# Performance work log

Hardware: AMD Instinct MI355X
Metric: run time of the kernel (lower is better)

Reference implementation:

```python
import jax, jax.numpy as jnp
import numpy as np

# Static config (init_kwargs)
H = 56; W = 56; C = 256; NH = 8; WS = 7; SS = 3
HD = C // NH
SCALE = HD ** -0.5
N = WS * WS                      # tokens per window = 49
NW = (H // WS) * (W // WS)       # windows per image = 64
HIDDEN = int(C * 4.0)
EPS = 1e-5


def _rel_pos_index():
    coords = np.stack(np.meshgrid(np.arange(WS), np.arange(WS), indexing='ij')).reshape(2, -1)
    rel = coords[:, :, None] - coords[:, None, :]          # [2, N, N]
    rel = rel.transpose(1, 2, 0).astype(np.int64)          # [N, N, 2]
    rel[:, :, 0] += WS - 1
    rel[:, :, 1] += WS - 1
    rel[:, :, 0] *= 2 * WS - 1
    return rel.sum(-1).reshape(-1)                         # [N*N]


def _attn_mask():
    # (0 / -100) mask for the shifted-window configuration, [NW, N, N]
    img = np.zeros([H, W])
    cnt = 0
    for hs in (slice(0, -WS), slice(-WS, -SS), slice(-SS, None)):
        for ws in (slice(0, -WS), slice(-WS, -SS), slice(-SS, None)):
            img[hs, ws] = cnt
            cnt += 1
    mw = img.reshape(H // WS, WS, W // WS, WS).transpose(0, 2, 1, 3).reshape(-1, N)
    diff = mw[:, None, :] - mw[:, :, None]                 # [NW, N, N]
    return np.where(diff != 0, -100.0, 0.0).astype(np.float32)


_REL_IDX = _rel_pos_index()
_MASK = _attn_mask()


def _ln(x, g, b):
    mu = jnp.mean(x, axis=-1, keepdims=True)
    var = jnp.mean((x - mu) ** 2, axis=-1, keepdims=True)
    return (x - mu) * jax.lax.rsqrt(var + EPS) * g + b


def setup_inputs() -> dict:
    key = jax.random.key(0)
    ks = jax.random.split(key, 16)
    B = 32
    s = 0.02
    return {
        'x': jax.random.normal(ks[0], (B, H * W, C), dtype=jnp.float32),
        'gamma1': jnp.ones((C,), jnp.float32),
        'beta1': jnp.zeros((C,), jnp.float32),
        'qkv_w': jax.random.normal(ks[1], (C, 3 * C), jnp.float32) * s,
        'qkv_b': jnp.zeros((3 * C,), jnp.float32),
        'proj_w': jax.random.normal(ks[2], (C, C), jnp.float32) * s,
        'proj_b': jnp.zeros((C,), jnp.float32),
        'rpb_table': jax.random.normal(ks[3], ((2 * WS - 1) * (2 * WS - 1), NH), jnp.float32) * s,
        'gamma2': jnp.ones((C,), jnp.float32),
        'beta2': jnp.zeros((C,), jnp.float32),
        'fc1_w': jax.random.normal(ks[4], (C, HIDDEN), jnp.float32) * s,
        'fc1_b': jnp.zeros((HIDDEN,), jnp.float32),
        'fc2_w': jax.random.normal(ks[5], (HIDDEN, C), jnp.float32) * s,
        'fc2_b': jnp.zeros((C,), jnp.float32),
    }


def reference(x, gamma1, beta1, qkv_w, qkv_b, proj_w, proj_b, rpb_table,
              gamma2, beta2, fc1_w, fc1_b, fc2_w, fc2_b):
    B = x.shape[0]
    y = _ln(x, gamma1, beta1).reshape(B, H, W, C)
    # cyclic shift
    y = jnp.roll(y, (-SS, -SS), axis=(1, 2))
    # window partition -> [B*NW, N, C]
    win = y.reshape(B, H // WS, WS, W // WS, WS, C)
    win = win.transpose(0, 1, 3, 2, 4, 5).reshape(-1, N, C)
    # qkv projection, split heads
    qkv = (win @ qkv_w + qkv_b).reshape(-1, N, 3, NH, HD).transpose(2, 0, 3, 1, 4)
    q, k, v = qkv[0] * SCALE, qkv[1], qkv[2]            # [B*NW, NH, N, HD]
    attn = jnp.einsum('bhnd,bhmd->bhnm', q, k)          # [B*NW, NH, N, N]
    # gathered relative position bias
    bias = rpb_table[jnp.asarray(_REL_IDX)].reshape(N, N, NH).transpose(2, 0, 1)
    attn = attn + bias[None]
    # shift mask
    mask = jnp.asarray(_MASK)                           # [NW, N, N]
    attn = attn.reshape(B, NW, NH, N, N) + mask[None, :, None]
    attn = jax.nn.softmax(attn.reshape(-1, NH, N, N), axis=-1)
    o = jnp.einsum('bhnm,bhmd->bnhd', attn, v).reshape(-1, N, C)
    o = o @ proj_w + proj_b
    # window reverse + reverse shift
    o = o.reshape(B, H // WS, W // WS, WS, WS, C).transpose(0, 1, 3, 2, 4, 5).reshape(B, H, W, C)
    o = jnp.roll(o, (SS, SS), axis=(1, 2)).reshape(B, H * W, C)
    x = x + o
    # MLP block
    y = _ln(x, gamma2, beta2)
    y = jax.nn.gelu(y @ fc1_w + fc1_b, approximate=False) @ fc2_w + fc2_b
    return x + y
```

## Files before the change

### kernel.cpp

```cpp
#include <hip/hip_runtime.h>
#include <hip/hip_bf16.h>
#include <math.h>


typedef __bf16 bf16_t;
typedef __bf16 bf16x4 __attribute__((ext_vector_type(4)));
typedef __bf16 bf16x8 __attribute__((ext_vector_type(8)));
typedef float f32x4 __attribute__((ext_vector_type(4)));

#define AS1 __attribute__((address_space(1)))
#define AS3 __attribute__((address_space(3)))

__device__ __forceinline__ void gload_lds16(const bf16_t* g, bf16_t* l) {
  __builtin_amdgcn_global_load_lds((AS1 void*)g, (AS3 void*)l, 16, 0, 0);
}

__global__ void transpose_cast3(const float* __restrict__ qkv_w,
                                const float* __restrict__ proj_w,
                                const float* __restrict__ fc1_w,
                                bf16_t* __restrict__ qkvWt,
                                bf16_t* __restrict__ projWt,
                                bf16_t* __restrict__ fc1Wt) {
  int idx = blockIdx.x * 256 + threadIdx.x;
  const float* w;
  bf16_t* wt;
  int N;
  if (blockIdx.y == 0) { w = qkv_w; wt = qkvWt; N = 768; }
  else if (blockIdx.y == 1) { w = proj_w; wt = projWt; N = 256; }
  else { w = fc1_w; wt = fc1Wt; N = 1024; }
  if (idx < N * 256) {
    int n = idx >> 8, k = idx & 255;
    wt[idx] = (bf16_t)w[(size_t)k * N + n];
  }
}

__global__ void transpose_cast(const float* __restrict__ w, bf16_t* __restrict__ wt,
                               int K, int N) {
  int idx = blockIdx.x * 256 + threadIdx.x;
  if (idx < N * K) {
    int n = idx / K, k = idx - n * K;
    wt[idx] = (bf16_t)w[(size_t)k * N + n];
  }
}

__global__ void build_bm(const float* __restrict__ rpb, float* __restrict__ bm) {
  int t = blockIdx.x, h = blockIdx.y;
  int wr = (t & 2) ? 7 : 0, wc = (t & 1) ? 7 : 0;
  for (int e = threadIdx.x; e < 4096; e += 256) {
    int r = e >> 6, c = e & 63;
    float v;
    if (c >= 49) {
      v = -30000.f;
    } else if (r >= 49) {
      v = 0.f;
    } else {
      int r1 = r / 7, c1 = r - r1 * 7;
      int r2 = c / 7, c2 = c - r2 * 7;
      v = rpb[((r1 - r2 + 6) * 13 + (c1 - c2 + 6)) * 8 + h];
      int hp = wr * 7 + r1, wp = wc * 7 + c1;
      int hq = wr * 7 + r2, wq = wc * 7 + c2;
      int ri = (hp < 49 ? 0 : (hp < 53 ? 1 : 2)) * 3 + (wp < 49 ? 0 : (wp < 53 ? 1 : 2));
      int rj = (hq < 49 ? 0 : (hq < 53 ? 1 : 2)) * 3 + (wq < 49 ? 0 : (wq < 53 ? 1 : 2));
      if (ri != rj) v -= 100.f;
    }
    bm[((size_t)(t * 8 + h) * 64 + r) * 64 + c] = v;
  }
}

__global__ __launch_bounds__(256)
void ln_cast(const float* __restrict__ src, const float* __restrict__ gamma,
             const float* __restrict__ beta, bf16_t* __restrict__ dst, int windowed) {
  int row = blockIdx.x * 4 + (threadIdx.x >> 6);
  int lane = threadIdx.x & 63;
  size_t srow;
  if (windowed) {
    int w = row / 49, t = row - w * 49;
    int img = w >> 6, wi = w & 63;
    int wr = wi >> 3, wc = wi & 7;
    int rr = t / 7, cc = t - rr * 7;
    int h = wr * 7 + rr + 3; if (h >= 56) h -= 56;
    int ww = wc * 7 + cc + 3; if (ww >= 56) ww -= 56;
    srow = (size_t)img * 3136 + h * 56 + ww;
  } else {
    srow = row;
  }
  float4 v = *(const float4*)(src + srow * 256 + lane * 4);
  float s = v.x + v.y + v.z + v.w;
  float s2 = v.x * v.x + v.y * v.y + v.z * v.z + v.w * v.w;
#pragma unroll
  for (int off = 32; off > 0; off >>= 1) {
    s += __shfl_xor(s, off);
    s2 += __shfl_xor(s2, off);
  }
  float mu = s * (1.0f / 256.0f);
  float rs = rsqrtf(s2 * (1.0f / 256.0f) - mu * mu + 1e-5f);
  float4 g = *(const float4*)(gamma + lane * 4);
  float4 b = *(const float4*)(beta + lane * 4);
  bf16x4 o;
  o[0] = (bf16_t)((v.x - mu) * rs * g.x + b.x);
  o[1] = (bf16_t)((v.y - mu) * rs * g.y + b.y);
  o[2] = (bf16_t)((v.z - mu) * rs * g.z + b.z);
  o[3] = (bf16_t)((v.w - mu) * rs * g.w + b.w);
  *(bf16x4*)(dst + (size_t)row * 256 + lane * 4) = o;
}

template <int MODE>
__global__ __launch_bounds__(256)
void gemm_bt(const bf16_t* __restrict__ A, const bf16_t* __restrict__ Bt,
             const float* __restrict__ bias,
             bf16_t* Cbf, float* Cf, const float* Res,
             int M, int N, int K) {
  __shared__ __align__(16) bf16_t As[128 * 32];
  __shared__ __align__(16) bf16_t Bs[128 * 32];
  const int tid = threadIdx.x;
  const int lane = tid & 63;
  const int wave = tid >> 6;
  const int wm = wave & 1, wn = wave >> 1;
  const int m0 = blockIdx.x * 128;
  const int n0 = blockIdx.y * 128;

  f32x4 acc[4][4];
#pragma unroll
  for (int i = 0; i < 4; i++)
#pragma unroll
    for (int j = 0; j < 4; j++) acc[i][j] = f32x4{0.f, 0.f, 0.f, 0.f};

  const bf16_t* Ag = A + (size_t)m0 * K;
  const bf16_t* Bg = Bt + (size_t)n0 * K;
  const int lr = lane & 15;
  const int kq = (lane >> 4) * 8;

  for (int k0 = 0; k0 < K; k0 += 32) {
#pragma unroll
    for (int it = 0; it < 2; it++) {
      int slot = it * 256 + tid;
      int row = slot >> 2;
      int ko = (slot & 3) << 3;
      bf16_t* ldsA = As + (it * 256 + wave * 64) * 8;
      bf16_t* ldsB = Bs + (it * 256 + wave * 64) * 8;
      gload_lds16(Ag + (size_t)row * K + k0 + ko, ldsA);
      gload_lds16(Bg + (size_t)row * K + k0 + ko, ldsB);
    }
    __syncthreads();
    bf16x8 af[4], bfr[4];
#pragma unroll
    for (int i = 0; i < 4; i++) {
      af[i]  = *(const bf16x8*)(As + (wm * 64 + i * 16 + lr) * 32 + kq);
      bfr[i] = *(const bf16x8*)(Bs + (wn * 64 + i * 16 + lr) * 32 + kq);
    }
#pragma unroll
    for (int i = 0; i < 4; i++)
#pragma unroll
      for (int j = 0; j < 4; j++)
        acc[i][j] = __builtin_amdgcn_mfma_f32_16x16x32_bf16(af[i], bfr[j], acc[i][j], 0, 0, 0);
    __syncthreads();
  }

  const int quad = lane >> 4;
#pragma unroll
  for (int i = 0; i < 4; i++) {
    int rbase = m0 + wm * 64 + i * 16 + quad * 4;
#pragma unroll
    for (int j = 0; j < 4; j++) {
      int col = n0 + wn * 64 + j * 16 + lr;
      float bi = bias[col];
#pragma unroll
      for (int r = 0; r < 4; r++) {
        int row = rbase + r;
        float v = acc[i][j][r] + bi;
        if (MODE == 0) {
          Cbf[(size_t)row * N + col] = (bf16_t)v;
        } else {
          int w = row / 49, t = row - w * 49;
          int img = w >> 6, wi = w & 63;
          int wr = wi >> 3, wc = wi & 7;
          int rr = t / 7, cc = t - rr * 7;
          int h = wr * 7 + rr + 3; if (h >= 56) h -= 56;
          int ww2 = wc * 7 + cc + 3; if (ww2 >= 56) ww2 -= 56;
          size_t idx = ((size_t)img * 3136 + h * 56 + ww2) * 256 + col;
          Cf[idx] = v + Res[idx];
        }
      }
    }
  }
}

__global__ __launch_bounds__(256)
void attn_mfma(const bf16_t* __restrict__ qkv, const float* __restrict__ bm,
               bf16_t* __restrict__ o) {
  __shared__ __align__(16) bf16_t Ps[64 * 72];
  __shared__ __align__(16) bf16_t Vt[32 * 72];
  const int w = blockIdx.x, h = blockIdx.y;
  const int tid = threadIdx.x;
  const int lane = tid & 63, wv = tid >> 6;
  const int lr = lane & 15, quad = lane >> 4;
  const int wi = w & 63;
  const int mtype = (((wi >> 3) == 7) ? 2 : 0) | (((wi & 7) == 7) ? 1 : 0);
  const bf16_t* base = qkv + (size_t)w * 49 * 768 + h * 32;

  bf16x8 zero8;
#pragma unroll
  for (int z = 0; z < 8; z++) zero8[z] = (bf16_t)0.f;

  {
    int tok = tid >> 2, d8 = (tid & 3) * 8;
    bf16x8 v8 = zero8;
    if (tok < 49) v8 = *(const bf16x8*)(base + (size_t)tok * 768 + 512 + d8);
#pragma unroll
    for (int z = 0; z < 8; z++) Vt[(d8 + z) * 72 + tok] = v8[z];
  }
  __syncthreads();

  const int mrow = 16 * wv + lr;
  bf16x8 aq = zero8;
  if (mrow < 49) aq = *(const bf16x8*)(base + (size_t)mrow * 768 + quad * 8);
  f32x4 s[4];
#pragma unroll
  for (int j = 0; j < 4; j++) {
    int nrow = 16 * j + lr;
    bf16x8 bk = zero8;
    if (nrow < 49) bk = *(const bf16x8*)(base + (size_t)nrow * 768 + 256 + quad * 8);
    s[j] = __builtin_amdgcn_mfma_f32_16x16x32_bf16(aq, bk, f32x4{0.f, 0.f, 0.f, 0.f}, 0, 0, 0);
  }

  const float* bmb = bm + ((size_t)(mtype * 8 + h) * 64 + 16 * wv) * 64;
  float inv[4];
#pragma unroll
  for (int reg = 0; reg < 4; reg++) {
    int rl = quad * 4 + reg;
    float v0[4];
    float mx = -1e30f;
#pragma unroll
    for (int j = 0; j < 4; j++) {
      float v = s[j][reg] * 0.17677669529663689f + bmb[rl * 64 + 16 * j + lr];
      v0[j] = v;
      mx = fmaxf(mx, v);
    }
#pragma unroll
    for (int off = 8; off > 0; off >>= 1) mx = fmaxf(mx, __shfl_xor(mx, off));
    float sum = 0.f;
#pragma unroll
    for (int j = 0; j < 4; j++) {
      float e = __expf(v0[j] - mx);
      v0[j] = e;
      sum += e;
    }
#pragma unroll
    for (int off = 8; off > 0; off >>= 1) sum += __shfl_xor(sum, off);
    inv[reg] = 1.0f / sum;
#pragma unroll
    for (int j = 0; j < 4; j++)
      Ps[(16 * wv + rl) * 72 + 16 * j + lr] = (bf16_t)v0[j];
  }

  f32x4 oacc[2];
  oacc[0] = f32x4{0.f, 0.f, 0.f, 0.f};
  oacc[1] = f32x4{0.f, 0.f, 0.f, 0.f};
#pragma unroll
  for (int kk = 0; kk < 2; kk++) {
    bf16x8 ap = *(const bf16x8*)(Ps + (16 * wv + lr) * 72 + kk * 32 + quad * 8);
#pragma unroll
    for (int n = 0; n < 2; n++) {
      bf16x8 bv = *(const bf16x8*)(Vt + (16 * n + lr) * 72 + kk * 32 + quad * 8);
      oacc[n] = __builtin_amdgcn_mfma_f32_16x16x32_bf16(ap, bv, oacc[n], 0, 0, 0);
    }
  }
#pragma unroll
  for (int n = 0; n < 2; n++) {
#pragma unroll
    for (int reg = 0; reg < 4; reg++) {
      int row = 16 * wv + quad * 4 + reg;
      if (row < 49) {
        int d = 16 * n + lr;
        o[((size_t)w * 49 + row) * 256 + h * 32 + d] = (bf16_t)(oacc[n][reg] * inv[reg]);
      }
    }
  }
}

__global__ __launch_bounds__(256, 2)
void fused_mlp(const bf16_t* __restrict__ y2, const bf16_t* __restrict__ W1t,
               const float* __restrict__ b1, const bf16_t* __restrict__ W2t,
               const float* __restrict__ b2, float* __restrict__ out) {
  __shared__ __align__(16) bf16_t Ls[64 * 264];
  __shared__ __align__(16) bf16_t Ws[8192];
  __shared__ __align__(16) bf16_t Hs[64 * 168];
  const int tid = threadIdx.x;
  const int lane = tid & 63, wave = tid >> 6;
  const int lr = lane & 15, quad = lane >> 4;
  const int wr = wave & 1, wc = wave >> 1;
  const int m0 = blockIdx.x * 64;

#pragma unroll
  for (int it = 0; it < 8; it++) {
    int slot = it * 256 + tid;
    int row = slot >> 5, g = slot & 31;
    bf16x8 v = *(const bf16x8*)(y2 + (size_t)(m0 + row) * 256 + g * 8);
    *(bf16x8*)(Ls + row * 264 + g * 8) = v;
  }
  __syncthreads();

  f32x4 acc2[2][8];
#pragma unroll
  for (int i = 0; i < 2; i++)
#pragma unroll
    for (int n = 0; n < 8; n++) acc2[i][n] = f32x4{0.f, 0.f, 0.f, 0.f};

  for (int hc = 0; hc < 8; hc++) {
    f32x4 acc1[2][4];
#pragma unroll
    for (int i = 0; i < 2; i++)
#pragma unroll
      for (int j = 0; j < 4; j++) acc1[i][j] = f32x4{0.f, 0.f, 0.f, 0.f};

    for (int ks = 0; ks < 4; ks++) {
      __syncthreads();
#pragma unroll
      for (int r = 0; r < 4; r++) {
        int sub = r >> 1, half = r & 1;
        int row = half * 64 + (tid >> 2), k8 = tid & 3;
        const bf16_t* src = W1t + (size_t)(hc * 128 + row) * 256 + ks * 64 + sub * 32 + k8 * 8;
        gload_lds16(src, Ws + sub * 4096 + half * 2048 + wave * 512);
      }
      __syncthreads();
#pragma unroll
      for (int kk = 0; kk < 2; kk++) {
        bf16x8 a[2], b[4];
#pragma unroll
        for (int i = 0; i < 2; i++)
          a[i] = *(const bf16x8*)(Ls + (32 * wr + 16 * i + lr) * 264 + ks * 64 + kk * 32 + quad * 8);
#pragma unroll
        for (int j = 0; j < 4; j++)
          b[j] = *(const bf16x8*)(Ws + kk * 4096 + (64 * wc + 16 * j + lr) * 32 + quad * 8);
#pragma unroll
        for (int i = 0; i < 2; i++)
#pragma unroll
          for (int j = 0; j < 4; j++)
            acc1[i][j] = __builtin_amdgcn_mfma_f32_16x16x32_bf16(a[i], b[j], acc1[i][j], 0, 0, 0);
      }
    }
#pragma unroll
    for (int i = 0; i < 2; i++) {
#pragma unroll
      for (int j = 0; j < 4; j++) {
        float bias1 = b1[hc * 128 + 64 * wc + 16 * j + lr];
        int hoff = (2 * wc + (j >> 1)) * 40 + (j & 1) * 16 + lr;
#pragma unroll
        for (int reg = 0; reg < 4; reg++) {
          int row_l = 32 * wr + 16 * i + quad * 4 + reg;
          float v = acc1[i][j][reg] + bias1;
          float arg = fminf(v * (0.7978845608f + 0.0356774081f * v * v), 15.f);
          float e = __expf(2.f * arg);
          float g = v * (e / (e + 1.f));
          Hs[row_l * 168 + hoff] = (bf16_t)g;
        }
      }
    }
    for (int ks2 = 0; ks2 < 4; ks2++) {
      __syncthreads();
#pragma unroll
      for (int r = 0; r < 4; r++) {
        int row = r * 64 + (tid >> 2), k8 = tid & 3;
        const bf16_t* src = W2t + (size_t)row * 1024 + hc * 128 + ks2 * 32 + k8 * 8;
        gload_lds16(src, Ws + r * 2048 + wave * 512);
      }
      __syncthreads();
      bf16x8 ah[2], bw[8];
#pragma unroll
      for (int i = 0; i < 2; i++)
        ah[i] = *(const bf16x8*)(Hs + (32 * wr + 16 * i + lr) * 168 + ks2 * 40 + quad * 8);
#pragma unroll
      for (int n = 0; n < 8; n++)
        bw[n] = *(const bf16x8*)(Ws + (128 * wc + 16 * n + lr) * 32 + quad * 8);
#pragma unroll
      for (int i = 0; i < 2; i++)
#pragma unroll
        for (int n = 0; n < 8; n++)
          acc2[i][n] = __builtin_amdgcn_mfma_f32_16x16x32_bf16(ah[i], bw[n], acc2[i][n], 0, 0, 0);
    }
  }

#pragma unroll
  for (int i = 0; i < 2; i++) {
#pragma unroll
    for (int n = 0; n < 8; n++) {
      int col = 128 * wc + 16 * n + lr;
      float bi = b2[col];
#pragma unroll
      for (int reg = 0; reg < 4; reg++) {
        int row = m0 + 32 * wr + 16 * i + quad * 4 + reg;
        size_t idx = (size_t)row * 256 + col;
        out[idx] = acc2[i][n][reg] + bi + out[idx];
      }
    }
  }
}

extern "C" void kernel_launch(void* const* d_in, const int* in_sizes, int n_in,
                              void* d_out, int out_size, void* d_ws, size_t ws_size,
                              hipStream_t stream) {
  const float* x      = (const float*)d_in[0];
  const float* g1     = (const float*)d_in[1];
  const float* b1     = (const float*)d_in[2];
  const float* qkv_w  = (const float*)d_in[3];
  const float* qkv_b  = (const float*)d_in[4];
  const float* proj_w = (const float*)d_in[5];
  const float* proj_b = (const float*)d_in[6];
  const float* rpb    = (const float*)d_in[7];
  const float* g2     = (const float*)d_in[8];
  const float* b2     = (const float*)d_in[9];
  const float* fc1_w  = (const float*)d_in[10];
  const float* fc1_b  = (const float*)d_in[11];
  const float* fc2_w  = (const float*)d_in[12];
  const float* fc2_b  = (const float*)d_in[13];
  float* out = (float*)d_out;
  char* ws = (char*)d_ws;

  bf16_t* xw   = (bf16_t*)ws;
  bf16_t* qkv  = (bf16_t*)(ws + 51380224);
  bf16_t* ow   = (bf16_t*)(ws + 205520896);
  bf16_t* y2   = xw;
  bf16_t* qkvWt  = (bf16_t*)(ws + 256901120);
  bf16_t* projWt = qkvWt + 768 * 256;
  bf16_t* fc1Wt  = projWt + 256 * 256;
  bf16_t* fc2Wt  = fc1Wt + 1024 * 256;
  float*  bm     = (float*)fc2Wt;

  transpose_cast3<<<dim3(1024, 3), 256, 0, stream>>>(qkv_w, proj_w, fc1_w,
                                                     qkvWt, projWt, fc1Wt);
  build_bm<<<dim3(4, 8), 256, 0, stream>>>(rpb, bm);

  ln_cast<<<25088, 256, 0, stream>>>(x, g1, b1, xw, 1);
  gemm_bt<0><<<dim3(784, 6), 256, 0, stream>>>(xw, qkvWt, qkv_b, qkv, nullptr, nullptr,
                                               100352, 768, 256);
  attn_mfma<<<dim3(2048, 8), 256, 0, stream>>>(qkv, bm, ow);
  transpose_cast<<<(256 * 1024 + 255) / 256, 256, 0, stream>>>(fc2_w, fc2Wt, 1024, 256);
  gemm_bt<3><<<dim3(784, 2), 256, 0, stream>>>(ow, projWt, proj_b, nullptr, out, x,
                                               100352, 256, 256);
  ln_cast<<<25088, 256, 0, stream>>>(out, g2, b2, y2, 0);
  fused_mlp<<<1568, 256, 0, stream>>>(y2, fc1Wt, fc1_b, fc2Wt, fc2_b, out);
}
```

Measured before the change: 800.8 us.

## Load MLP A operand from global, shrink LDS, raise occupancy, linearize GEMM grid

The fused MLP kernel no longer stages the 64x256 input tile in LDS. Each wave reads its A fragments straight from global memory, the hidden buffer shrinks to a 136 stride, and launch bounds are raised to 3 blocks per CU to improve occupancy. Separately, the GEMM grid is flattened to 1D with N-major block ordering, so blocks sharing an A tile run back to back and reuse it in L2. The risks are repeated global loads of A across the outer hidden-chunk loop, register pressure under the tighter launch bound, and possible LDS bank conflicts from the new stride.

Measured after the change: 828.9 us. +3.5%, slower.

```diff
diff --git a/kernel.cpp b/kernel.cpp
--- a/kernel.cpp
+++ b/kernel.cpp
@@ -109,15 +109,18 @@
 void gemm_bt(const bf16_t* __restrict__ A, const bf16_t* __restrict__ Bt,
              const float* __restrict__ bias,
              bf16_t* Cbf, float* Cf, const float* Res,
-             int M, int N, int K) {
+             int M, int N, int K, int nblk) {
   __shared__ __align__(16) bf16_t As[128 * 32];
   __shared__ __align__(16) bf16_t Bs[128 * 32];
   const int tid = threadIdx.x;
   const int lane = tid & 63;
   const int wave = tid >> 6;
   const int wm = wave & 1, wn = wave >> 1;
-  const int m0 = blockIdx.x * 128;
-  const int n0 = blockIdx.y * 128;
+  const int bid = blockIdx.x;
+  const int m_idx = bid / nblk;
+  const int n_idx = bid - m_idx * nblk;
+  const int m0 = m_idx * 128;
+  const int n0 = n_idx * 128;
 
   f32x4 acc[4][4];
 #pragma unroll
@@ -278,27 +281,19 @@
   }
 }
 
-__global__ __launch_bounds__(256, 2)
+__global__ __launch_bounds__(256, 3)
 void fused_mlp(const bf16_t* __restrict__ y2, const bf16_t* __restrict__ W1t,
                const float* __restrict__ b1, const bf16_t* __restrict__ W2t,
                const float* __restrict__ b2, float* __restrict__ out) {
-  __shared__ __align__(16) bf16_t Ls[64 * 264];
   __shared__ __align__(16) bf16_t Ws[8192];
-  __shared__ __align__(16) bf16_t Hs[64 * 168];
+  __shared__ __align__(16) bf16_t Hs[64 * 136];
   const int tid = threadIdx.x;
   const int lane = tid & 63, wave = tid >> 6;
   const int lr = lane & 15, quad = lane >> 4;
   const int wr = wave & 1, wc = wave >> 1;
   const int m0 = blockIdx.x * 64;
-
-#pragma unroll
-  for (int it = 0; it < 8; it++) {
-    int slot = it * 256 + tid;
-    int row = slot >> 5, g = slot & 31;
-    bf16x8 v = *(const bf16x8*)(y2 + (size_t)(m0 + row) * 256 + g * 8);
-    *(bf16x8*)(Ls + row * 264 + g * 8) = v;
-  }
-  __syncthreads();
+  const bf16_t* Arow0 = y2 + (size_t)(m0 + 32 * wr + lr) * 256;
+  const bf16_t* Arow1 = y2 + (size_t)(m0 + 32 * wr + 16 + lr) * 256;
 
   f32x4 acc2[2][8];
 #pragma unroll
@@ -322,13 +317,16 @@
         const bf16_t* src = W1t + (size_t)(hc * 128 + row) * 256 + ks * 64 + sub * 32 + k8 * 8;
         gload_lds16(src, Ws + sub * 4096 + half * 2048 + wave * 512);
       }
+      bf16x8 a[2][2];
+#pragma unroll
+      for (int kk = 0; kk < 2; kk++) {
+        a[kk][0] = *(const bf16x8*)(Arow0 + ks * 64 + kk * 32 + quad * 8);
+        a[kk][1] = *(const bf16x8*)(Arow1 + ks * 64 + kk * 32 + quad * 8);
+      }
       __syncthreads();
 #pragma unroll
       for (int kk = 0; kk < 2; kk++) {
-        bf16x8 a[2], b[4];
-#pragma unroll
-        for (int i = 0; i < 2; i++)
-          a[i] = *(const bf16x8*)(Ls + (32 * wr + 16 * i + lr) * 264 + ks * 64 + kk * 32 + quad * 8);
+        bf16x8 b[4];
 #pragma unroll
         for (int j = 0; j < 4; j++)
           b[j] = *(const bf16x8*)(Ws + kk * 4096 + (64 * wc + 16 * j + lr) * 32 + quad * 8);
@@ -336,7 +334,7 @@
         for (int i = 0; i < 2; i++)
 #pragma unroll
           for (int j = 0; j < 4; j++)
-            acc1[i][j] = __builtin_amdgcn_mfma_f32_16x16x32_bf16(a[i], b[j], acc1[i][j], 0, 0, 0);
+            acc1[i][j] = __builtin_amdgcn_mfma_f32_16x16x32_bf16(a[kk][i], b[j], acc1[i][j], 0, 0, 0);
       }
     }
 #pragma unroll
@@ -344,7 +342,7 @@
 #pragma unroll
       for (int j = 0; j < 4; j++) {
         float bias1 = b1[hc * 128 + 64 * wc + 16 * j + lr];
-        int hoff = (2 * wc + (j >> 1)) * 40 + (j & 1) * 16 + lr;
+        int hcol = 64 * wc + 16 * j + lr;
 #pragma unroll
         for (int reg = 0; reg < 4; reg++) {
           int row_l = 32 * wr + 16 * i + quad * 4 + reg;
@@ -352,7 +350,7 @@
           float arg = fminf(v * (0.7978845608f + 0.0356774081f * v * v), 15.f);
           float e = __expf(2.f * arg);
           float g = v * (e / (e + 1.f));
-          Hs[row_l * 168 + hoff] = (bf16_t)g;
+          Hs[row_l * 136 + hcol] = (bf16_t)g;
         }
       }
     }
@@ -368,7 +366,7 @@
       bf16x8 ah[2], bw[8];
 #pragma unroll
       for (int i = 0; i < 2; i++)
-        ah[i] = *(const bf16x8*)(Hs + (32 * wr + 16 * i + lr) * 168 + ks2 * 40 + quad * 8);
+        ah[i] = *(const bf16x8*)(Hs + (32 * wr + 16 * i + lr) * 136 + ks2 * 32 + quad * 8);
 #pragma unroll
       for (int n = 0; n < 8; n++)
         bw[n] = *(const bf16x8*)(Ws + (128 * wc + 16 * n + lr) * 32 + quad * 8);
@@ -431,12 +429,12 @@
   build_bm<<<dim3(4, 8), 256, 0, stream>>>(rpb, bm);
 
   ln_cast<<<25088, 256, 0, stream>>>(x, g1, b1, xw, 1);
-  gemm_bt<0><<<dim3(784, 6), 256, 0, stream>>>(xw, qkvWt, qkv_b, qkv, nullptr, nullptr,
-                                               100352, 768, 256);
+  gemm_bt<0><<<784 * 6, 256, 0, stream>>>(xw, qkvWt, qkv_b, qkv, nullptr, nullptr,
+                                          100352, 768, 256, 6);
   attn_mfma<<<dim3(2048, 8), 256, 0, stream>>>(qkv, bm, ow);
   transpose_cast<<<(256 * 1024 + 255) / 256, 256, 0, stream>>>(fc2_w, fc2Wt, 1024, 256);
-  gemm_bt<3><<<dim3(784, 2), 256, 0, stream>>>(ow, projWt, proj_b, nullptr, out, x,
-                                               100352, 256, 256);
+  gemm_bt<3><<<784 * 2, 256, 0, stream>>>(ow, projWt, proj_b, nullptr, out, x,
+                                          100352, 256, 256, 2);
   ln_cast<<<25088, 256, 0, stream>>>(out, g2, b2, y2, 0);
   fused_mlp<<<1568, 256, 0, stream>>>(y2, fc1Wt, fc1_b, fc2Wt, fc2_b, out);
 }
```
